# Kernel optimization log

Hardware: AMD Instinct MI355X
Metric: run time of the kernel (lower is better)

The kernel has to match this reference:

```python
import jax, jax.numpy as jnp
import numpy as np

N_NODES = 200000
N_EDGES = 6400000
IN_F, HID, OUT = 28, 16, 2


def setup_inputs() -> dict:
    key = jax.random.key(0)
    k1, k2, k3, k4 = jax.random.split(key, 4)
    x = jax.random.normal(k1, (N_NODES, IN_F), dtype=jnp.float32)
    edge_index = jax.random.randint(k2, (2, N_EDGES), 0, N_NODES, dtype=jnp.int64)
    # Glorot-ish init for the two GCNConv weights
    W1 = jax.random.normal(k3, (IN_F, HID), dtype=jnp.float32) / np.sqrt(IN_F)
    b1 = jnp.zeros((HID,), dtype=jnp.float32)
    W2 = jax.random.normal(k4, (HID, OUT), dtype=jnp.float32) / np.sqrt(HID)
    b2 = jnp.zeros((OUT,), dtype=jnp.float32)
    return {"x": x, "edge_index": edge_index, "W1": W1, "b1": b1, "W2": W2, "b2": b2}


def _gcn_conv(h, W, b, src, dst, n_nodes):
    # PyG GCNConv: h' = D^{-1/2} (A + I) D^{-1/2} (h W) + b, self-loops already in src/dst
    h = h @ W  # [N, F_out] — transform first (small F), then aggregate
    deg = jax.ops.segment_sum(jnp.ones_like(dst, dtype=h.dtype), dst, num_segments=n_nodes)
    dis = jnp.where(deg > 0, jax.lax.rsqrt(jnp.maximum(deg, 1.0)), 0.0)
    norm = dis[src] * dis[dst]                    # [E]
    msg = h[src] * norm[:, None]                  # gather + scale
    agg = jax.ops.segment_sum(msg, dst, num_segments=n_nodes)  # scatter-add
    return agg + b


def reference(x, edge_index, W1, b1, W2, b2):
    n = x.shape[0]
    loops = jnp.arange(n, dtype=edge_index.dtype)
    src = jnp.concatenate([edge_index[0], loops])  # add self-loops
    dst = jnp.concatenate([edge_index[1], loops])
    h = _gcn_conv(x, W1, b1, src, dst, n)
    h = jax.nn.relu(h)
    # F.dropout(training=self.training): inference mode -> identity
    h = _gcn_conv(h, W2, b2, src, dst, n)
    return jax.nn.log_softmax(h, axis=1)
```

## Files before the change

kernel.cpp:

```cpp
#include <hip/hip_runtime.h>
#include <hip/hip_fp16.h>
#include <math.h>

#define N_IN_F 28
#define N_HID 16
#define NPB 256
#define NBK 1024
#define EPB 8192
#define SRC_BITS 18
#define SRC_MASK ((1 << SRC_BITS) - 1)
#define STAGE_CAP 10240


__global__ void __launch_bounds__(512)
k_bhist(const int* __restrict__ dst, unsigned short* __restrict__ chunk_hist, int ne) {
    __shared__ int hist[NBK];
    int tid = threadIdx.x;
    for (int t = tid; t < NBK; t += 512) hist[t] = 0;
    __syncthreads();
    int e0 = blockIdx.x * EPB;
    int e1 = min(e0 + EPB, ne);
    for (int e = e0 + tid; e < e1; e += 512) atomicAdd(&hist[dst[e] >> 8], 1);
    __syncthreads();
    unsigned short* ch = chunk_hist + (size_t)blockIdx.x * NBK;
    for (int t = tid; t < NBK; t += 512) ch[t] = (unsigned short)hist[t];
}

__global__ void __launch_bounds__(256)
k_colscan(const unsigned short* __restrict__ chunk_hist, int* __restrict__ gdelta,
          int* __restrict__ total, int nchunk) {
    __shared__ int p[16][17];
    int tid = threadIdx.x;
    int j = tid & 15;
    int g = tid >> 4;
    int bkt = blockIdx.x * 16 + j;
    int cpg = (nchunk + 15) >> 4;
    int c0 = g * cpg, c1 = min(c0 + cpg, nchunk);

    int s = 0;
    for (int c = c0; c < c1; ++c) s += chunk_hist[(size_t)c * NBK + bkt];
    p[g][j] = s;
    __syncthreads();

    if (tid < 16) {
        int run = 0;
#pragma unroll
        for (int gg = 0; gg < 16; ++gg) { int t = p[gg][tid]; p[gg][tid] = run; run += t; }
        total[blockIdx.x * 16 + tid] = run;
    }
    __syncthreads();

    int run = p[g][j];
    for (int c = c0; c < c1; ++c) {
        int h = chunk_hist[(size_t)c * NBK + bkt];
        gdelta[(size_t)c * NBK + bkt] = run;
        run += h;
    }
}

__global__ void k_top(const int* __restrict__ total, int* __restrict__ base, int ne) {
    __shared__ int sm[NBK];
    int tid = threadIdx.x;
    int v = total[tid];
    sm[tid] = v;
    __syncthreads();
    for (int off = 1; off < NBK; off <<= 1) {
        int t = (tid >= off) ? sm[tid - off] : 0;
        __syncthreads();
        sm[tid] += t;
        __syncthreads();
    }
    base[tid] = sm[tid] - v;
    if (tid == 0) base[NBK] = ne;
}

__global__ void __launch_bounds__(1024)
k_bin(const int* __restrict__ src, const int* __restrict__ dst,
      const unsigned short* __restrict__ chunk_hist, const int* __restrict__ gdelta,
      const int* __restrict__ base, int* __restrict__ binned, int ne) {
    __shared__ int gpos[NBK];
    __shared__ int lcur[NBK];
    __shared__ int wpart[16];
    __shared__ int stage[EPB];
    __shared__ unsigned short sbid[EPB];
    int tid = threadIdx.x;
    int lane = tid & 63;
    int wid = tid >> 6;
    int chunk = blockIdx.x;

    int h = chunk_hist[(size_t)chunk * NBK + tid];
    int val = h;
#pragma unroll
    for (int off = 1; off < 64; off <<= 1) {
        int t = __shfl_up(val, off, 64);
        if (lane >= off) val += t;
    }
    if (lane == 63) wpart[wid] = val;
    __syncthreads();
    if (wid == 0) {
        int p = (lane < 16) ? wpart[lane] : 0;
#pragma unroll
        for (int off = 1; off < 16; off <<= 1) {
            int t = __shfl_up(p, off, 64);
            if (lane >= off) p += t;
        }
        if (lane < 16) wpart[lane] = p;
    }
    __syncthreads();
    int wbase = (wid > 0) ? wpart[wid - 1] : 0;
    int excl = wbase + val - h;
    gpos[tid] = base[tid] + gdelta[(size_t)chunk * NBK + tid] - excl;
    lcur[tid] = excl;
    __syncthreads();

    int e0 = chunk * EPB;
    int csz = min(EPB, ne - e0);

    for (int i = tid; i < csz; i += 1024) {
        int d = dst[e0 + i];
        int b = d >> 8;
        int r = atomicAdd(&lcur[b], 1);
        stage[r] = src[e0 + i] | ((d & (NPB - 1)) << SRC_BITS);
        sbid[r] = (unsigned short)b;
    }
    __syncthreads();

    for (int i = tid; i < csz; i += 1024) {
        binned[gpos[sbid[i]] + i] = stage[i];
    }
}

__global__ void __launch_bounds__(512)
k_sort2(const int* __restrict__ base, const int* __restrict__ binned,
        int* __restrict__ binned2, int* __restrict__ row_start,
        float* __restrict__ dis, const float* __restrict__ x,
        const float* __restrict__ W1, __half* __restrict__ hs1_lo,
        __half* __restrict__ hs1_hi, int n, int nb_total) {
    __shared__ int cnt[NPB];
    __shared__ int pos[NPB];
    __shared__ int cur[NPB];
    __shared__ float w[N_IN_F * N_HID];
    __shared__ int stage[STAGE_CAP];
    int tid = threadIdx.x;
    if (tid < NPB) cnt[tid] = 0;
    for (int t = tid; t < N_IN_F * N_HID; t += 512) w[t] = W1[t];
    __syncthreads();

    int b = blockIdx.x;
    int e0 = base[b], e1 = base[b + 1];
    int csz = e1 - e0;

    for (int e = e0 + tid; e < e1; e += 512) atomicAdd(&cnt[binned[e] >> SRC_BITS], 1);
    __syncthreads();

    int v = (tid < NPB) ? cnt[tid] : 0;
    if (tid < NPB) pos[tid] = v;
    __syncthreads();
    for (int off = 1; off < NPB; off <<= 1) {
        int t = (tid < NPB && tid >= off) ? pos[tid - off] : 0;
        __syncthreads();
        if (tid < NPB) pos[tid] += t;
        __syncthreads();
    }
    if (tid < NPB) {
        int excl = pos[tid] - v;
        cur[tid] = excl;
        int g = b * NPB + tid;
        if (g < n) {
            row_start[g] = e0 + excl;
            dis[g] = rsqrtf((float)(v + 1));
        }
    }
    if (b == nb_total - 1 && tid == 0) row_start[n] = e1;
    __syncthreads();

    for (int e = e0 + tid; e < e1; e += 512) {
        int p = binned[e];
        int r = atomicAdd(&cur[p >> SRC_BITS], 1);
        int val = p & SRC_MASK;
        if (r < STAGE_CAP) stage[r] = val;
        else binned2[e0 + r] = val;
    }
    __syncthreads();

    int lim = min(csz, STAGE_CAP);
    for (int i = tid; i < lim; i += 512) binned2[e0 + i] = stage[i];

    if (tid < NPB) {
        int g = b * NPB + tid;
        if (g < n) {
            float di = rsqrtf((float)(cnt[tid] + 1));
            float xi[N_IN_F];
            const float4* xr = (const float4*)(x + (size_t)g * N_IN_F);
#pragma unroll
            for (int q = 0; q < N_IN_F / 4; ++q) {
                float4 vv = xr[q];
                xi[4 * q + 0] = vv.x; xi[4 * q + 1] = vv.y;
                xi[4 * q + 2] = vv.z; xi[4 * q + 3] = vv.w;
            }
            __half2 hp[N_HID / 2];
#pragma unroll
            for (int f2 = 0; f2 < N_HID / 2; ++f2) {
                float ha = 0.0f, hb = 0.0f;
#pragma unroll
                for (int k = 0; k < N_IN_F; ++k) {
                    ha = fmaf(xi[k], w[k * N_HID + 2 * f2], ha);
                    hb = fmaf(xi[k], w[k * N_HID + 2 * f2 + 1], hb);
                }
                hp[f2] = __floats2half2_rn(ha * di, hb * di);
            }
            ((int4*)hs1_lo)[g] = *(const int4*)&hp[0];
            ((int4*)hs1_hi)[g] = *(const int4*)&hp[4];
        }
    }
}


template <int FH>
__global__ void __launch_bounds__(256)
k_agg1h(const int* __restrict__ row_start, const int* __restrict__ esrc,
        const __half2* __restrict__ tbl, const float* __restrict__ dis,
        const float* __restrict__ b1, const float* __restrict__ W2,
        float2* __restrict__ hs2p, float2* __restrict__ hs2, int n) {
    int t = blockIdx.x * blockDim.x + threadIdx.x;
    int node = t >> 2;
    int f2 = t & 3;
    if (node >= n) return;

    int beg = row_start[node];
    int end = row_start[node + 1];
    const __half2* H = tbl + f2;

    float2 sl = __half22float2(H[node * 4]);
    float ax = sl.x, ay = sl.y;
    float a0x = 0.f, a0y = 0.f, a1x = 0.f, a1y = 0.f;
    float a2x = 0.f, a2y = 0.f, a3x = 0.f, a3y = 0.f;
    int j = beg;
    for (; j + 8 <= end; j += 8) {
        int s0 = esrc[j],     s1 = esrc[j + 1], s2 = esrc[j + 2], s3 = esrc[j + 3];
        int s4 = esrc[j + 4], s5 = esrc[j + 5], s6 = esrc[j + 6], s7 = esrc[j + 7];
        float2 v0 = __half22float2(H[s0 * 4]);
        float2 v1 = __half22float2(H[s1 * 4]);
        float2 v2 = __half22float2(H[s2 * 4]);
        float2 v3 = __half22float2(H[s3 * 4]);
        float2 v4 = __half22float2(H[s4 * 4]);
        float2 v5 = __half22float2(H[s5 * 4]);
        float2 v6 = __half22float2(H[s6 * 4]);
        float2 v7 = __half22float2(H[s7 * 4]);
        a0x += v0.x; a0y += v0.y; a1x += v1.x; a1y += v1.y;
        a2x += v2.x; a2y += v2.y; a3x += v3.x; a3y += v3.y;
        a0x += v4.x; a0y += v4.y; a1x += v5.x; a1y += v5.y;
        a2x += v6.x; a2y += v6.y; a3x += v7.x; a3y += v7.y;
    }
    for (; j + 4 <= end; j += 4) {
        int s0 = esrc[j], s1 = esrc[j + 1], s2 = esrc[j + 2], s3 = esrc[j + 3];
        float2 v0 = __half22float2(H[s0 * 4]);
        float2 v1 = __half22float2(H[s1 * 4]);
        float2 v2 = __half22float2(H[s2 * 4]);
        float2 v3 = __half22float2(H[s3 * 4]);
        a0x += v0.x; a0y += v0.y; a1x += v1.x; a1y += v1.y;
        a2x += v2.x; a2y += v2.y; a3x += v3.x; a3y += v3.y;
    }
    for (; j < end; ++j) {
        float2 v0 = __half22float2(H[esrc[j] * 4]);
        ax += v0.x; ay += v0.y;
    }
    ax += (a0x + a1x) + (a2x + a3x);
    ay += (a0y + a1y) + (a2y + a3y);

    float di = dis[node];
    int feat = FH * 8 + 2 * f2;
    float vx = fmaxf(fmaf(di, ax, b1[feat + 0]), 0.0f);
    float vy = fmaxf(fmaf(di, ay, b1[feat + 1]), 0.0f);
    float c0 = vx * W2[2 * feat + 0] + vy * W2[2 * feat + 2];
    float c1 = vx * W2[2 * feat + 1] + vy * W2[2 * feat + 3];
#pragma unroll
    for (int off = 2; off > 0; off >>= 1) {
        c0 += __shfl_xor(c0, off, 4);
        c1 += __shfl_xor(c1, off, 4);
    }
    if (f2 == 0) {
        if (FH == 0) {
            float2 o; o.x = c0; o.y = c1;
            hs2p[node] = o;
        } else {
            float2 p = hs2p[node];
            float2 o;
            o.x = (p.x + c0) * di;
            o.y = (p.y + c1) * di;
            hs2[node] = o;
        }
    }
}

__global__ void __launch_bounds__(256)
k_agg2(const int* __restrict__ row_start, const int* __restrict__ esrc,
       const float2* __restrict__ hs2, const float* __restrict__ dis,
       const float* __restrict__ b2, float2* __restrict__ out, int n) {
    int t = blockIdx.x * blockDim.x + threadIdx.x;
    int node = t >> 2;
    int l = t & 3;
    if (node >= n) return;

    int beg = row_start[node];
    int end = row_start[node + 1];
    float cx = 0.f, cy = 0.f, dx = 0.f, dy = 0.f;
    int j = beg + l;
    for (; j + 4 < end; j += 8) {
        int s0 = esrc[j];
        int s1 = esrc[j + 4];
        float2 v0 = hs2[s0];
        float2 v1 = hs2[s1];
        cx += v0.x; cy += v0.y;
        dx += v1.x; dy += v1.y;
    }
    if (j < end) {
        float2 v = hs2[esrc[j]];
        cx += v.x; cy += v.y;
    }
    cx += dx; cy += dy;
#pragma unroll
    for (int off = 2; off > 0; off >>= 1) {
        cx += __shfl_xor(cx, off, 4);
        cy += __shfl_xor(cy, off, 4);
    }
    if (l == 0) {
        float2 self = hs2[node];
        float di = dis[node];
        float a = fmaf(di, cx + self.x, b2[0]);
        float c = fmaf(di, cy + self.y, b2[1]);
        float m = fmaxf(a, c);
        float lse = m + logf(expf(a - m) + expf(c - m));
        float2 o;
        o.x = a - lse;
        o.y = c - lse;
        out[node] = o;
    }
}


extern "C" void kernel_launch(void* const* d_in, const int* in_sizes, int n_in,
                              void* d_out, int out_size, void* d_ws, size_t ws_size,
                              hipStream_t stream) {
    const float* x  = (const float*)d_in[0];
    const int*   ei = (const int*)d_in[1];
    const float* W1 = (const float*)d_in[2];
    const float* b1 = (const float*)d_in[3];
    const float* W2 = (const float*)d_in[4];
    const float* b2 = (const float*)d_in[5];
    float2* out = (float2*)d_out;

    const int n  = in_sizes[0] / N_IN_F;
    const int ne = in_sizes[1] / 2;
    const int* src = ei;
    const int* dst = ei + ne;
    const int nb = (n + NPB - 1) / NPB;
    const int nchunk = (ne + EPB - 1) / EPB;

    int* ws_i = (int*)d_ws;
    int* total     = ws_i;
    int* base      = total + 1024;
    int* row_start = base + 1028;
    float* dis     = (float*)(row_start + n + 4);
    float2* hs2    = (float2*)(dis + n);
    float2* hs2p   = hs2 + n;
    __half* hs1_lo = (__half*)(hs2p + n);
    __half* hs1_hi = hs1_lo + 8 * (size_t)n;
    unsigned short* chunk_hist = (unsigned short*)(hs1_hi + 8 * (size_t)n);
    int* binned2   = (int*)chunk_hist + ((size_t)nchunk * NBK + 1) / 2;
    int* binned    = binned2 + ne;
    int* gdelta    = binned2;

    const int B = 256;

    k_bhist<<<dim3(nchunk), dim3(512), 0, stream>>>(dst, chunk_hist, ne);
    k_colscan<<<dim3(NBK / 16), dim3(B), 0, stream>>>(chunk_hist, gdelta, total, nchunk);
    k_top<<<dim3(1), dim3(NBK), 0, stream>>>(total, base, ne);
    k_bin<<<dim3(nchunk), dim3(1024), 0, stream>>>(src, dst, chunk_hist, gdelta, base, binned, ne);
    k_sort2<<<dim3(nb), dim3(512), 0, stream>>>(base, binned, binned2, row_start, dis,
                                                x, W1, hs1_lo, hs1_hi, n, nb);
    {
        long long tot = (long long)n * 4;
        unsigned nbk = (unsigned)((tot + B - 1) / B);
        k_agg1h<0><<<dim3(nbk), dim3(B), 0, stream>>>(
            row_start, binned2, (const __half2*)hs1_lo, dis, b1, W2, hs2p, hs2, n);
        k_agg1h<1><<<dim3(nbk), dim3(B), 0, stream>>>(
            row_start, binned2, (const __half2*)hs1_hi, dis, b1, W2, hs2p, hs2, n);
        k_agg2<<<dim3(nbk), dim3(B), 0, stream>>>(
            row_start, binned2, hs2, dis, b2, out, n);
    }
}
```

Measured before the change: 207.5 us.

## Merge split half-precision feature tables into one 32-byte row and fuse aggregation passes

Interleaves the two 8-feature half tables into a single 16-feature row per node and replaces the two per-half layer-1 aggregation kernels with one kernel that uses 8 lanes per node. This halves the reads of the edge-index list and removes the partial hs2p round trip and one launch. The inner gather loop is also unrolled to 16 edges. In exchange, the gathered table is twice as large (6.4MB), so it fits L2 less easily than the split 3.2MB halves the earlier code was likely built around.

```diff
diff --git a/kernel.cpp b/kernel.cpp
--- a/kernel.cpp
+++ b/kernel.cpp
@@ -134,8 +134,8 @@
 k_sort2(const int* __restrict__ base, const int* __restrict__ binned,
         int* __restrict__ binned2, int* __restrict__ row_start,
         float* __restrict__ dis, const float* __restrict__ x,
-        const float* __restrict__ W1, __half* __restrict__ hs1_lo,
-        __half* __restrict__ hs1_hi, int n, int nb_total) {
+        const float* __restrict__ W1, __half* __restrict__ hs1,
+        int n, int nb_total) {
     __shared__ int cnt[NPB];
     __shared__ int pos[NPB];
     __shared__ int cur[NPB];
@@ -209,87 +209,79 @@
                 }
                 hp[f2] = __floats2half2_rn(ha * di, hb * di);
             }
-            ((int4*)hs1_lo)[g] = *(const int4*)&hp[0];
-            ((int4*)hs1_hi)[g] = *(const int4*)&hp[4];
+            int4* dstp = (int4*)(hs1 + (size_t)g * N_HID);
+            dstp[0] = *(const int4*)&hp[0];
+            dstp[1] = *(const int4*)&hp[4];
         }
     }
 }
 
 
-template <int FH>
 __global__ void __launch_bounds__(256)
-k_agg1h(const int* __restrict__ row_start, const int* __restrict__ esrc,
-        const __half2* __restrict__ tbl, const float* __restrict__ dis,
-        const float* __restrict__ b1, const float* __restrict__ W2,
-        float2* __restrict__ hs2p, float2* __restrict__ hs2, int n) {
+k_agg1(const int* __restrict__ row_start, const int* __restrict__ esrc,
+       const __half2* __restrict__ hs1, const float* __restrict__ dis,
+       const float* __restrict__ b1, const float* __restrict__ W2,
+       float2* __restrict__ hs2, int n) {
     int t = blockIdx.x * blockDim.x + threadIdx.x;
-    int node = t >> 2;
-    int f2 = t & 3;
+    int node = t >> 3;
+    int f2 = t & 7;
     if (node >= n) return;
 
     int beg = row_start[node];
     int end = row_start[node + 1];
-    const __half2* H = tbl + f2;
-
-    float2 sl = __half22float2(H[node * 4]);
+    const __half2* H = hs1 + f2;
+
+    float2 sl = __half22float2(H[node * 8]);
     float ax = sl.x, ay = sl.y;
     float a0x = 0.f, a0y = 0.f, a1x = 0.f, a1y = 0.f;
     float a2x = 0.f, a2y = 0.f, a3x = 0.f, a3y = 0.f;
     int j = beg;
-    for (; j + 8 <= end; j += 8) {
-        int s0 = esrc[j],     s1 = esrc[j + 1], s2 = esrc[j + 2], s3 = esrc[j + 3];
-        int s4 = esrc[j + 4], s5 = esrc[j + 5], s6 = esrc[j + 6], s7 = esrc[j + 7];
-        float2 v0 = __half22float2(H[s0 * 4]);
-        float2 v1 = __half22float2(H[s1 * 4]);
-        float2 v2 = __half22float2(H[s2 * 4]);
-        float2 v3 = __half22float2(H[s3 * 4]);
-        float2 v4 = __half22float2(H[s4 * 4]);
-        float2 v5 = __half22float2(H[s5 * 4]);
-        float2 v6 = __half22float2(H[s6 * 4]);
-        float2 v7 = __half22float2(H[s7 * 4]);
+    for (; j + 16 <= end; j += 16) {
+        int s[16];
+#pragma unroll
+        for (int q = 0; q < 16; ++q) s[q] = esrc[j + q];
+        float2 v[16];
+#pragma unroll
+        for (int q = 0; q < 16; ++q) v[q] = __half22float2(H[s[q] * 8]);
+#pragma unroll
+        for (int q = 0; q < 16; q += 4) {
+            a0x += v[q + 0].x; a0y += v[q + 0].y;
+            a1x += v[q + 1].x; a1y += v[q + 1].y;
+            a2x += v[q + 2].x; a2y += v[q + 2].y;
+            a3x += v[q + 3].x; a3y += v[q + 3].y;
+        }
+    }
+    for (; j + 4 <= end; j += 4) {
+        int s0 = esrc[j], s1 = esrc[j + 1], s2 = esrc[j + 2], s3 = esrc[j + 3];
+        float2 v0 = __half22float2(H[s0 * 8]);
+        float2 v1 = __half22float2(H[s1 * 8]);
+        float2 v2 = __half22float2(H[s2 * 8]);
+        float2 v3 = __half22float2(H[s3 * 8]);
         a0x += v0.x; a0y += v0.y; a1x += v1.x; a1y += v1.y;
         a2x += v2.x; a2y += v2.y; a3x += v3.x; a3y += v3.y;
-        a0x += v4.x; a0y += v4.y; a1x += v5.x; a1y += v5.y;
-        a2x += v6.x; a2y += v6.y; a3x += v7.x; a3y += v7.y;
-    }
-    for (; j + 4 <= end; j += 4) {
-        int s0 = esrc[j], s1 = esrc[j + 1], s2 = esrc[j + 2], s3 = esrc[j + 3];
-        float2 v0 = __half22float2(H[s0 * 4]);
-        float2 v1 = __half22float2(H[s1 * 4]);
-        float2 v2 = __half22float2(H[s2 * 4]);
-        float2 v3 = __half22float2(H[s3 * 4]);
-        a0x += v0.x; a0y += v0.y; a1x += v1.x; a1y += v1.y;
-        a2x += v2.x; a2y += v2.y; a3x += v3.x; a3y += v3.y;
     }
     for (; j < end; ++j) {
-        float2 v0 = __half22float2(H[esrc[j] * 4]);
+        float2 v0 = __half22float2(H[esrc[j] * 8]);
         ax += v0.x; ay += v0.y;
     }
     ax += (a0x + a1x) + (a2x + a3x);
     ay += (a0y + a1y) + (a2y + a3y);
 
     float di = dis[node];
-    int feat = FH * 8 + 2 * f2;
-    float vx = fmaxf(fmaf(di, ax, b1[feat + 0]), 0.0f);
-    float vy = fmaxf(fmaf(di, ay, b1[feat + 1]), 0.0f);
-    float c0 = vx * W2[2 * feat + 0] + vy * W2[2 * feat + 2];
-    float c1 = vx * W2[2 * feat + 1] + vy * W2[2 * feat + 3];
-#pragma unroll
-    for (int off = 2; off > 0; off >>= 1) {
-        c0 += __shfl_xor(c0, off, 4);
-        c1 += __shfl_xor(c1, off, 4);
+    float vx = fmaxf(fmaf(di, ax, b1[2 * f2 + 0]), 0.0f);
+    float vy = fmaxf(fmaf(di, ay, b1[2 * f2 + 1]), 0.0f);
+    float c0 = vx * W2[4 * f2 + 0] + vy * W2[4 * f2 + 2];
+    float c1 = vx * W2[4 * f2 + 1] + vy * W2[4 * f2 + 3];
+#pragma unroll
+    for (int off = 4; off > 0; off >>= 1) {
+        c0 += __shfl_xor(c0, off, 8);
+        c1 += __shfl_xor(c1, off, 8);
     }
     if (f2 == 0) {
-        if (FH == 0) {
-            float2 o; o.x = c0; o.y = c1;
-            hs2p[node] = o;
-        } else {
-            float2 p = hs2p[node];
-            float2 o;
-            o.x = (p.x + c0) * di;
-            o.y = (p.y + c1) * di;
-            hs2[node] = o;
-        }
+        float2 o;
+        o.x = c0 * di;
+        o.y = c1 * di;
+        hs2[node] = o;
     }
 }
 
@@ -363,10 +355,8 @@
     int* row_start = base + 1028;
     float* dis     = (float*)(row_start + n + 4);
     float2* hs2    = (float2*)(dis + n);
-    float2* hs2p   = hs2 + n;
-    __half* hs1_lo = (__half*)(hs2p + n);
-    __half* hs1_hi = hs1_lo + 8 * (size_t)n;
-    unsigned short* chunk_hist = (unsigned short*)(hs1_hi + 8 * (size_t)n);
+    __half* hs1    = (__half*)(hs2 + n);
+    unsigned short* chunk_hist = (unsigned short*)((int*)hs1 + 8 * (size_t)n);
     int* binned2   = (int*)chunk_hist + ((size_t)nchunk * NBK + 1) / 2;
     int* binned    = binned2 + ne;
     int* gdelta    = binned2;
@@ -378,15 +368,15 @@
     k_top<<<dim3(1), dim3(NBK), 0, stream>>>(total, base, ne);
     k_bin<<<dim3(nchunk), dim3(1024), 0, stream>>>(src, dst, chunk_hist, gdelta, base, binned, ne);
     k_sort2<<<dim3(nb), dim3(512), 0, stream>>>(base, binned, binned2, row_start, dis,
-                                                x, W1, hs1_lo, hs1_hi, n, nb);
+                                                x, W1, hs1, n, nb);
+    {
+        long long tot = (long long)n * 8;
+        k_agg1<<<dim3((unsigned)((tot + B - 1) / B)), dim3(B), 0, stream>>>(
+            row_start, binned2, (const __half2*)hs1, dis, b1, W2, hs2, n);
+    }
     {
         long long tot = (long long)n * 4;
-        unsigned nbk = (unsigned)((tot + B - 1) / B);
-        k_agg1h<0><<<dim3(nbk), dim3(B), 0, stream>>>(
-            row_start, binned2, (const __half2*)hs1_lo, dis, b1, W2, hs2p, hs2, n);
-        k_agg1h<1><<<dim3(nbk), dim3(B), 0, stream>>>(
-            row_start, binned2, (const __half2*)hs1_hi, dis, b1, W2, hs2p, hs2, n);
-        k_agg2<<<dim3(nbk), dim3(B), 0, stream>>>(
+        k_agg2<<<dim3((unsigned)((tot + B - 1) / B)), dim3(B), 0, stream>>>(
             row_start, binned2, hs2, dis, b2, out, n);
     }
 }
```

Result: faster. 181.5 us (-12.5%).
